# Optimization experiments

Hardware: AMD Instinct MI355X
Metric: run time of the kernel (lower is better)

The kernel has to match this reference:

```python
import jax, jax.numpy as jnp
import numpy as np
import math

# Static module config (matches init_kwargs)
C = 1.0            # ball curvature parameter c
IN_C, OUT_C = 512, 512
K, PAD = 3, 1
T, B = 2048, 16
EPS = 1e-15
RC = math.sqrt(C)

def _beta(a, b):
    return math.exp(math.lgamma(a) + math.lgamma(b) - math.lgamma(a + b))

BETA_NI = _beta(IN_C / 2.0, 0.5)            # beta(n_i/2, 1/2)
BETA_N = _beta(IN_C * K / 2.0, 0.5)         # beta(n/2, 1/2)
BETA_RATIO = BETA_N / BETA_NI
PROJ_EPS = 4e-3                              # geoopt float32 projection eps


def logmap0(y):
    # y in Poincare ball -> tangent at origin
    yn = jnp.clip(jnp.linalg.norm(y, axis=-1, keepdims=True), EPS, None)
    arg = jnp.clip(RC * yn, None, 1.0 - 1e-7)
    return y * (jnp.arctanh(arg) / (RC * yn))


def expmap0(u):
    un = jnp.clip(jnp.linalg.norm(u, axis=-1, keepdims=True), EPS, None)
    return jnp.tanh(RC * un) * u / (RC * un)


def project(x):
    maxnorm = (1.0 - PROJ_EPS) / RC
    norm = jnp.clip(jnp.linalg.norm(x, axis=-1, keepdims=True), EPS, None)
    return x * jnp.where(norm > maxnorm, maxnorm / norm, 1.0)


def poincare_linear(x, w_g, w_unit, b):
    # unidirectional Poincare MLR (geoopt_plusplus)
    rcx = RC * x                                             # [T,B,K*Cin]
    cx2 = jnp.sum(rcx * rcx, axis=-1, keepdims=True)         # [T,B,1]
    drcr = 2.0 * RC * b                                      # [Cout]
    num = 2.0 * jnp.einsum('tbi,io->tbo', rcx, w_unit) * jnp.cosh(drcr) \
          - (1.0 + cx2) * jnp.sinh(drcr)
    y = (2.0 * w_g / RC) * jnp.arcsinh(num / jnp.clip(1.0 - cx2, EPS, None))
    y = jnp.sinh(RC * y) / RC
    denom = 1.0 + jnp.sqrt(1.0 + C * jnp.sum(y * y, axis=-1, keepdims=True))
    return project(y / denom)


def setup_inputs() -> dict:
    key = jax.random.key(0)
    k1, k2, k3 = jax.random.split(key, 3)
    # points strictly inside the unit ball: ||x|| < 0.7
    v = jax.random.normal(k1, (T, B, IN_C), dtype=jnp.float32)
    vn = jnp.linalg.norm(v, axis=-1, keepdims=True)
    x = v / (1.0 + vn) * 0.7
    std = (2.0 * IN_C * K * OUT_C) ** -0.5
    w = jax.random.normal(k2, (K * IN_C, OUT_C), dtype=jnp.float32) * std
    weight_g = jnp.clip(jnp.linalg.norm(w, axis=0), 1e-15, None)   # [Cout]
    weight_v = w / weight_g                                        # [K*Cin, Cout]
    bias = jnp.zeros((OUT_C,), dtype=jnp.float32)
    return {"x": x, "weight_g": weight_g, "weight_v": weight_v, "bias": bias}


def reference(x, weight_g, weight_v, bias):
    u = logmap0(x) * BETA_RATIO                 # tangent space, rescaled
    u = jnp.pad(u, ((PAD, PAD), (0, 0), (0, 0)))
    olen = u.shape[0] - K + 1
    # im2col over time: [olen, B, K*Cin]
    u = jnp.concatenate([u[k:k + olen] for k in range(K)], axis=-1)
    xh = expmap0(u)
    w_unit = weight_v / jnp.clip(jnp.linalg.norm(weight_v, axis=0), EPS, None)
    return poincare_linear(xh, weight_g, w_unit, bias)
```

## Files before the change

### kernel.cpp

```cpp
#include <hip/hip_runtime.h>
#include <cstdint>
#include <cmath>

typedef unsigned short u16;
typedef short bf16x8 __attribute__((ext_vector_type(8)));
typedef float f32x4 __attribute__((ext_vector_type(4)));

#define T_DIM 2048
#define B_DIM 16
#define CIN 512
#define COUT 512
#define KIN 1536
#define NROWS (T_DIM * B_DIM)
#define UROWS ((T_DIM + 2) * B_DIM)

#define BM 128
#define BK 64
#define NT (KIN / BK)

#define LOG2E 1.44269504088896f
#define LN2   0.69314718055995f

__device__ __forceinline__ float fast_exp2(float x) {
#if __has_builtin(__builtin_amdgcn_exp2f)
  return __builtin_amdgcn_exp2f(x);
#else
  return __builtin_exp2f(x);
#endif
}
__device__ __forceinline__ float fast_log2(float x) {
#if __has_builtin(__builtin_amdgcn_logf)
  return __builtin_amdgcn_logf(x);
#else
  return __builtin_log2f(x);
#endif
}
__device__ __forceinline__ float fast_rcp(float x) {
  return __builtin_amdgcn_rcpf(x);
}

__device__ __forceinline__ u16 f2bf(float f) {
  unsigned u = __builtin_bit_cast(unsigned, f);
  u = (u + 0x7FFFu + ((u >> 16) & 1u)) >> 16;
  return (u16)u;
}

typedef __attribute__((address_space(3))) unsigned int as3u32;
typedef __attribute__((address_space(1))) unsigned int as1u32;

__device__ __forceinline__ void gload16(const u16* g, const u16* lds) {
#if __has_builtin(__builtin_amdgcn_global_load_lds)
  __builtin_amdgcn_global_load_lds((as1u32*)(uintptr_t)g,
                                   (as3u32*)(unsigned)(uintptr_t)lds, 16, 0, 0);
#else
  unsigned lane = __lane_id();
  ((uint4*)lds)[lane] = *(const uint4*)g;
#endif
}

__global__ __launch_bounds__(256) void k_colnorm(const float* __restrict__ wv,
                                                 float* __restrict__ partial) {
  int o = blockIdx.x * 256 + threadIdx.x;
  int r0 = blockIdx.y * 64;
  float s = 0.f;
#pragma unroll 8
  for (int r = 0; r < 64; ++r) {
    float v = wv[(size_t)(r0 + r) * COUT + o];
    s += v * v;
  }
  partial[(size_t)blockIdx.y * COUT + o] = s;
}

__global__ __launch_bounds__(256) void k_fin(const float* __restrict__ partial,
                                             float* __restrict__ invn) {
  int o = blockIdx.x * 256 + threadIdx.x;
  float s = 0.f;
#pragma unroll
  for (int j = 0; j < KIN / 64; ++j) s += partial[(size_t)j * COUT + o];
  invn[o] = 1.f / fmaxf(sqrtf(s), 1e-15f);
}

__global__ void k_chsh(const float* __restrict__ bias, float* __restrict__ ch,
                       float* __restrict__ sh) {
  int o = blockIdx.x * blockDim.x + threadIdx.x;
  if (o < COUT) {
    float d = 2.f * bias[o];
    float e = fast_exp2(d * LOG2E);
    float ie = fast_rcp(e);
    ch[o] = 0.5f * (e + ie);
    sh[o] = 0.5f * (e - ie);
  }
}

__global__ void k_wt(const float* __restrict__ wv, const float* __restrict__ invn,
                     u16* __restrict__ wt) {
  __shared__ float tile[64][65];
  int i0 = blockIdx.x * 64;
  int o0 = blockIdx.y * 64;
  int tx = threadIdx.x & 63, ty = threadIdx.x >> 6;
  for (int r = ty; r < 64; r += 4)
    tile[r][tx] = wv[(size_t)(i0 + r) * COUT + o0 + tx];
  __syncthreads();
  for (int r = ty; r < 64; r += 4) {
    float inv = invn[o0 + r];
    wt[(size_t)(o0 + r) * KIN + i0 + tx] = f2bf(tile[tx][r] * inv);
  }
}

__global__ void k_logmap(const float* __restrict__ x, u16* __restrict__ U,
                         float* __restrict__ nsq, float beta_ratio) {
  int row = blockIdx.x;
  int t = row >> 4;
  int lane = threadIdx.x;
  uint4* urow = (uint4*)(U + (size_t)row * CIN);
  if (t == 0 || t == T_DIM + 1) {
    uint4 z; z.x = z.y = z.z = z.w = 0u;
    urow[lane] = z;
    if (lane == 0) nsq[row] = 0.f;
    return;
  }
  const float4* xr = (const float4*)(x + (size_t)(row - 16) * CIN);
  float4 a = xr[lane * 2];
  float4 b = xr[lane * 2 + 1];
  float s = a.x*a.x + a.y*a.y + a.z*a.z + a.w*a.w
          + b.x*b.x + b.y*b.y + b.z*b.z + b.w*b.w;
#pragma unroll
  for (int d = 1; d < 64; d <<= 1) s += __shfl_xor(s, d);
  float r = sqrtf(s);
  float yn = fmaxf(r, 1e-15f);
  float arg = fminf(yn, 1.0f - 1e-7f);
  float at = 0.5f * LN2 * fast_log2((1.f + arg) * fast_rcp(1.f - arg));
  float f = at / yn * beta_ratio;
  union { u16 h[8]; uint4 v; } pk;
  pk.h[0] = f2bf(a.x * f); pk.h[1] = f2bf(a.y * f);
  pk.h[2] = f2bf(a.z * f); pk.h[3] = f2bf(a.w * f);
  pk.h[4] = f2bf(b.x * f); pk.h[5] = f2bf(b.y * f);
  pk.h[6] = f2bf(b.z * f); pk.h[7] = f2bf(b.w * f);
  urow[lane] = pk.v;
  if (lane == 0) nsq[row] = s * f * f;
}

__global__ __launch_bounds__(256) void k_rows(const float* __restrict__ nsq,
                                              float* __restrict__ R1,
                                              float* __restrict__ R2) {
  int m = blockIdx.x * 256 + threadIdx.x;
  float un2 = nsq[m] + nsq[m + 16] + nsq[m + 32];
  float un = sqrtf(un2);
  float unc = fmaxf(un, 1e-15f);
  float e2 = fast_exp2(unc * (2.f * LOG2E));
  float th = (e2 - 1.f) * fast_rcp(e2 + 1.f);
  float sxp = th * fast_rcp(unc);
  float cx2 = sxp * sxp * un2;
  float iden = fast_rcp(fmaxf(1.f - cx2, 1e-15f));
  R1[m] = 2.f * sxp * iden;
  R2[m] = (1.f + cx2) * iden;
}

__global__ __launch_bounds__(512, 2) void k_gemm(const u16* __restrict__ U,
                                                 const u16* __restrict__ WT,
                                                 const float* __restrict__ R1,
                                                 const float* __restrict__ R2,
                                                 const float* __restrict__ wg,
                                                 const float* __restrict__ chv,
                                                 const float* __restrict__ shv,
                                                 float* __restrict__ out) {
  __shared__ u16 lA[2][BM * BK];
  __shared__ u16 lB[COUT * BK];
  int bm = blockIdx.x;
  int tid = threadIdx.x;
  int lane = tid & 63;
  int wid = tid >> 6;
  int wr = wid >> 2, wc = wid & 3;
  int lr = lane & 15;
  int srow = tid >> 3;
  int chSw = (tid & 7) ^ (srow & 7);
  int pc0 = (((lane >> 4)) ^ (lr & 7)) << 3;
  int pc1 = (((lane >> 4) | 4) ^ (lr & 7)) << 3;

  f32x4 acc[4][8] = {};

  auto STAGE_A = [&](int t, int p) {
    int seg = t >> 3;
    int c0 = (t & 7) << 6;
    const u16* gA = U + (size_t)(bm * BM + seg * 16) * 512 + c0 + chSw * 8;
#pragma unroll
    for (int r = 0; r < 2; ++r) {
      int row = r * 64 + srow;
      gload16(gA + (size_t)row * 512, &lA[p][(r * 64 + wid * 8) * BK]);
    }
  };
  auto STAGE_B = [&](int t) {
    const u16* gB = WT + (size_t)t * 64 + chSw * 8;
#pragma unroll
    for (int r = 0; r < 8; ++r) {
      int row = r * 64 + srow;
      gload16(gB + (size_t)row * KIN, &lB[(r * 64 + wid * 8) * BK]);
    }
  };

  STAGE_A(0, 0);
  STAGE_B(0);
  asm volatile("s_waitcnt vmcnt(0)" ::: "memory");
  asm volatile("s_barrier" ::: "memory");

  for (int t = 0; t < NT; ++t) {
    int p = t & 1;
    if (t < NT - 1) STAGE_A(t + 1, p ^ 1);
    const u16* pA = &lA[p][(wr * 64 + lr) * BK];
    const u16* pB = &lB[(wc * 128 + lr) * BK];
#pragma unroll
    for (int kk = 0; kk < 2; ++kk) {
      int pc = kk ? pc1 : pc0;
      bf16x8 af[4], bf[8];
#pragma unroll
      for (int i = 0; i < 4; ++i) af[i] = *(const bf16x8*)(pA + i * 16 * BK + pc);
#pragma unroll
      for (int i = 0; i < 8; ++i) bf[i] = *(const bf16x8*)(pB + i * 16 * BK + pc);
      __builtin_amdgcn_s_setprio(1);
#pragma unroll
      for (int mi = 0; mi < 4; ++mi)
#pragma unroll
        for (int ni = 0; ni < 8; ++ni)
          acc[mi][ni] = __builtin_amdgcn_mfma_f32_16x16x32_bf16(
              af[mi], bf[ni], acc[mi][ni], 0, 0, 0);
      __builtin_amdgcn_s_setprio(0);
    }
    asm volatile("s_waitcnt lgkmcnt(0)" ::: "memory");
    asm volatile("s_barrier" ::: "memory");
    if (t < NT - 1) {
      STAGE_B(t + 1);
      asm volatile("s_waitcnt vmcnt(0)" ::: "memory");
      asm volatile("s_barrier" ::: "memory");
    }
  }
  float* scr = (float*)&lA[0][0];
  float* scl = scr + 128 * 4;

  float g8[8], c8[8], s8[8];
#pragma unroll
  for (int ni = 0; ni < 8; ++ni) {
    int col = wc * 128 + ni * 16 + lr;
    g8[ni] = wg[col]; c8[ni] = chv[col]; s8[ni] = shv[col];
  }

  int rbase_loc = wr * 64 + ((lane >> 4) << 2);
  int rbase_glb = bm * BM + rbase_loc;

#pragma unroll
  for (int mi = 0; mi < 4; ++mi) {
    float4 r1v = *(const float4*)(R1 + rbase_glb + mi * 16);
    float4 r2v = *(const float4*)(R2 + rbase_glb + mi * 16);
    float r1a[4] = {r1v.x, r1v.y, r1v.z, r1v.w};
    float r2a[4] = {r2v.x, r2v.y, r2v.z, r2v.w};
    float ssq[4] = {0.f, 0.f, 0.f, 0.f};
#pragma unroll
    for (int ni = 0; ni < 8; ++ni) {
#pragma unroll
      for (int j = 0; j < 4; ++j) {
        float z = r1a[j] * acc[mi][ni][j] * c8[ni] - r2a[j] * s8[ni];
        float w = z + sqrtf(fmaf(z, z, 1.f));
        float l = fast_log2(w);
        float E = fast_exp2((2.f * g8[ni]) * l);
        float y = 0.5f * (E - fast_rcp(E));
        acc[mi][ni][j] = y;
        ssq[j] += y * y;
      }
    }
#pragma unroll
    for (int j = 0; j < 4; ++j) {
#pragma unroll
      for (int d = 1; d < 16; d <<= 1) ssq[j] += __shfl_xor(ssq[j], d);
    }
    if (lr == 0) {
#pragma unroll
      for (int j = 0; j < 4; ++j)
        scr[(rbase_loc + mi * 16 + j) * 4 + wc] = ssq[j];
    }
  }
  __syncthreads();
  if (tid < 128) {
    float ss = scr[tid * 4] + scr[tid * 4 + 1] + scr[tid * 4 + 2] + scr[tid * 4 + 3];
    float denom = 1.f + sqrtf(1.f + ss);
    float idn = 1.f / denom;
    float nrm = fmaxf(sqrtf(ss) * idn, 1e-15f);
    float maxn = 1.0f - 4e-3f;
    float scale = (nrm > maxn) ? (maxn / nrm) : 1.f;
    scl[tid] = scale * idn;
  }
  __syncthreads();

#pragma unroll
  for (int mi = 0; mi < 4; ++mi) {
    float sc[4];
#pragma unroll
    for (int j = 0; j < 4; ++j) sc[j] = scl[rbase_loc + mi * 16 + j];
#pragma unroll
    for (int ni = 0; ni < 8; ++ni) {
      int col = wc * 128 + ni * 16 + lr;
#pragma unroll
      for (int j = 0; j < 4; ++j)
        out[(size_t)(rbase_glb + mi * 16 + j) * COUT + col] = acc[mi][ni][j] * sc[j];
    }
  }
}

extern "C" void kernel_launch(void* const* d_in, const int* in_sizes, int n_in,
                              void* d_out, int out_size, void* d_ws, size_t ws_size,
                              hipStream_t stream) {
  const float* x    = (const float*)d_in[0];
  const float* wg   = (const float*)d_in[1];
  const float* wv   = (const float*)d_in[2];
  const float* bias = (const float*)d_in[3];
  float* out = (float*)d_out;

  char* ws = (char*)d_ws;
  u16*   U    = (u16*)(ws);
  float* NSQ  = (float*)(ws + 33587200);
  u16*   WT   = (u16*)(ws + 33718400);
  float* INVN = (float*)(ws + 35291264);
  float* CH   = (float*)(ws + 35293312);
  float* SH   = (float*)(ws + 35295360);
  float* PART = (float*)(ws + 35297408);
  float* R1   = (float*)(ws + 35346560);
  float* R2   = (float*)(ws + 35477632);

  double lb = (lgamma(768.0) + lgamma(0.5) - lgamma(768.5))
            - (lgamma(256.0) + lgamma(0.5) - lgamma(256.5));
  float beta_ratio = (float)exp(lb);

  k_colnorm<<<dim3(COUT / 256, KIN / 64), 256, 0, stream>>>(wv, PART);
  k_fin<<<COUT / 256, 256, 0, stream>>>(PART, INVN);
  k_chsh<<<COUT / 128, 128, 0, stream>>>(bias, CH, SH);
  k_wt<<<dim3(KIN / 64, COUT / 64), 256, 0, stream>>>(wv, INVN, WT);
  k_logmap<<<UROWS, 64, 0, stream>>>(x, U, NSQ, beta_ratio);
  k_rows<<<NROWS / 256, 256, 0, stream>>>(NSQ, R1, R2);
  k_gemm<<<NROWS / BM, 512, 0, stream>>>(U, WT, R1, R2, wg, CH, SH, out);
}
```

Baseline: 116.7 us.

## Triple-buffer A and B tiles in GEMM and fold row/bias kernels into neighbors

The GEMM main loop moves from BK=64 with double-buffered A and a single B buffer (two barriers per step) to BK=32 with three rotating buffers for both A and B. Loads run two stages ahead and each step uses one barrier with a partial vmcnt wait. The k_rows kernel is removed and its per-row tanh/denominator math is recomputed in the GEMM epilogue from nsq. k_chsh is merged into k_fin, cutting two launches. The cost is three times as many pipeline steps with smaller MFMA bursts per barrier and some extra epilogue work.

```diff
diff --git a/kernel.cpp b/kernel.cpp
--- a/kernel.cpp
+++ b/kernel.cpp
@@ -14,9 +14,7 @@
 #define NROWS (T_DIM * B_DIM)
 #define UROWS ((T_DIM + 2) * B_DIM)
 
-#define BM 128
-#define BK 64
-#define NT (KIN / BK)
+#define NS 48
 
 #define LOG2E 1.44269504088896f
 #define LN2   0.69314718055995f
@@ -72,24 +70,20 @@
 }
 
 __global__ __launch_bounds__(256) void k_fin(const float* __restrict__ partial,
-                                             float* __restrict__ invn) {
+                                             const float* __restrict__ bias,
+                                             float* __restrict__ invn,
+                                             float* __restrict__ ch,
+                                             float* __restrict__ sh) {
   int o = blockIdx.x * 256 + threadIdx.x;
   float s = 0.f;
 #pragma unroll
   for (int j = 0; j < KIN / 64; ++j) s += partial[(size_t)j * COUT + o];
   invn[o] = 1.f / fmaxf(sqrtf(s), 1e-15f);
-}
-
-__global__ void k_chsh(const float* __restrict__ bias, float* __restrict__ ch,
-                       float* __restrict__ sh) {
-  int o = blockIdx.x * blockDim.x + threadIdx.x;
-  if (o < COUT) {
-    float d = 2.f * bias[o];
-    float e = fast_exp2(d * LOG2E);
-    float ie = fast_rcp(e);
-    ch[o] = 0.5f * (e + ie);
-    sh[o] = 0.5f * (e - ie);
-  }
+  float d = 2.f * bias[o];
+  float e = fast_exp2(d * LOG2E);
+  float ie = fast_rcp(e);
+  ch[o] = 0.5f * (e + ie);
+  sh[o] = 0.5f * (e - ie);
 }
 
 __global__ void k_wt(const float* __restrict__ wv, const float* __restrict__ invn,
@@ -140,82 +134,58 @@
   if (lane == 0) nsq[row] = s * f * f;
 }
 
-__global__ __launch_bounds__(256) void k_rows(const float* __restrict__ nsq,
-                                              float* __restrict__ R1,
-                                              float* __restrict__ R2) {
-  int m = blockIdx.x * 256 + threadIdx.x;
-  float un2 = nsq[m] + nsq[m + 16] + nsq[m + 32];
-  float un = sqrtf(un2);
-  float unc = fmaxf(un, 1e-15f);
-  float e2 = fast_exp2(unc * (2.f * LOG2E));
-  float th = (e2 - 1.f) * fast_rcp(e2 + 1.f);
-  float sxp = th * fast_rcp(unc);
-  float cx2 = sxp * sxp * un2;
-  float iden = fast_rcp(fmaxf(1.f - cx2, 1e-15f));
-  R1[m] = 2.f * sxp * iden;
-  R2[m] = (1.f + cx2) * iden;
-}
-
 __global__ __launch_bounds__(512, 2) void k_gemm(const u16* __restrict__ U,
                                                  const u16* __restrict__ WT,
-                                                 const float* __restrict__ R1,
-                                                 const float* __restrict__ R2,
+                                                 const float* __restrict__ nsq,
                                                  const float* __restrict__ wg,
                                                  const float* __restrict__ chv,
                                                  const float* __restrict__ shv,
                                                  float* __restrict__ out) {
-  __shared__ u16 lA[2][BM * BK];
-  __shared__ u16 lB[COUT * BK];
+  __shared__ u16 lA[3][128 * 32];
+  __shared__ u16 lB[3][512 * 32];
   int bm = blockIdx.x;
   int tid = threadIdx.x;
   int lane = tid & 63;
   int wid = tid >> 6;
   int wr = wid >> 2, wc = wid & 3;
   int lr = lane & 15;
-  int srow = tid >> 3;
-  int chSw = (tid & 7) ^ (srow & 7);
-  int pc0 = (((lane >> 4)) ^ (lr & 7)) << 3;
-  int pc1 = (((lane >> 4) | 4) ^ (lr & 7)) << 3;
+  int sc = (tid & 3) ^ ((tid >> 3) & 3);
+  int cSwz = ((lane >> 4) ^ ((lr >> 1) & 3)) << 3;
 
   f32x4 acc[4][8] = {};
 
-  auto STAGE_A = [&](int t, int p) {
-    int seg = t >> 3;
-    int c0 = (t & 7) << 6;
-    const u16* gA = U + (size_t)(bm * BM + seg * 16) * 512 + c0 + chSw * 8;
-#pragma unroll
-    for (int r = 0; r < 2; ++r) {
-      int row = r * 64 + srow;
-      gload16(gA + (size_t)row * 512, &lA[p][(r * 64 + wid * 8) * BK]);
-    }
+  auto stgA = [&](int t, int p) {
+    int seg = t >> 4;
+    int c0 = (t & 15) << 5;
+    gload16(U + (size_t)(bm * 128 + seg * 16 + (tid >> 2)) * 512 + c0 + sc * 8,
+            &lA[p][wid * 512]);
   };
-  auto STAGE_B = [&](int t) {
-    const u16* gB = WT + (size_t)t * 64 + chSw * 8;
-#pragma unroll
-    for (int r = 0; r < 8; ++r) {
-      int row = r * 64 + srow;
-      gload16(gB + (size_t)row * KIN, &lB[(r * 64 + wid * 8) * BK]);
-    }
+  auto stgB = [&](int t, int p) {
+#pragma unroll
+    for (int r = 0; r < 4; ++r)
+      gload16(WT + (size_t)(r * 128 + (tid >> 2)) * KIN + t * 32 + sc * 8,
+              &lB[p][r * 4096 + wid * 512]);
   };
 
-  STAGE_A(0, 0);
-  STAGE_B(0);
-  asm volatile("s_waitcnt vmcnt(0)" ::: "memory");
+  stgA(0, 0); stgB(0, 0);
+  stgA(1, 1); stgB(1, 1);
+  asm volatile("s_waitcnt vmcnt(5)" ::: "memory");
   asm volatile("s_barrier" ::: "memory");
 
-  for (int t = 0; t < NT; ++t) {
-    int p = t & 1;
-    if (t < NT - 1) STAGE_A(t + 1, p ^ 1);
-    const u16* pA = &lA[p][(wr * 64 + lr) * BK];
-    const u16* pB = &lB[(wc * 128 + lr) * BK];
-#pragma unroll
-    for (int kk = 0; kk < 2; ++kk) {
-      int pc = kk ? pc1 : pc0;
+  for (int tt = 0; tt < 16; ++tt) {
+#pragma unroll
+    for (int u = 0; u < 3; ++u) {
+      int t = tt * 3 + u;
+      int b = u;
+      int p = (u + 2) % 3;
+      if (t + 2 < NS) { stgA(t + 2, p); stgB(t + 2, p); }
+      const u16* pA = &lA[b][(wr * 64 + lr) * 32 + cSwz];
+      const u16* pB = &lB[b][(wc * 128 + lr) * 32 + cSwz];
       bf16x8 af[4], bf[8];
 #pragma unroll
-      for (int i = 0; i < 4; ++i) af[i] = *(const bf16x8*)(pA + i * 16 * BK + pc);
-#pragma unroll
-      for (int i = 0; i < 8; ++i) bf[i] = *(const bf16x8*)(pB + i * 16 * BK + pc);
+      for (int i = 0; i < 4; ++i) af[i] = *(const bf16x8*)(pA + i * 512);
+#pragma unroll
+      for (int i = 0; i < 8; ++i) bf[i] = *(const bf16x8*)(pB + i * 512);
       __builtin_amdgcn_s_setprio(1);
 #pragma unroll
       for (int mi = 0; mi < 4; ++mi)
@@ -224,15 +194,13 @@
           acc[mi][ni] = __builtin_amdgcn_mfma_f32_16x16x32_bf16(
               af[mi], bf[ni], acc[mi][ni], 0, 0, 0);
       __builtin_amdgcn_s_setprio(0);
-    }
-    asm volatile("s_waitcnt lgkmcnt(0)" ::: "memory");
-    asm volatile("s_barrier" ::: "memory");
-    if (t < NT - 1) {
-      STAGE_B(t + 1);
-      asm volatile("s_waitcnt vmcnt(0)" ::: "memory");
+      asm volatile("s_waitcnt lgkmcnt(0)" ::: "memory");
+      if (t < NS - 2)       asm volatile("s_waitcnt vmcnt(5)" ::: "memory");
+      else if (t == NS - 2) asm volatile("s_waitcnt vmcnt(0)" ::: "memory");
       asm volatile("s_barrier" ::: "memory");
     }
   }
+
   float* scr = (float*)&lA[0][0];
   float* scl = scr + 128 * 4;
 
@@ -242,17 +210,27 @@
     int col = wc * 128 + ni * 16 + lr;
     g8[ni] = wg[col]; c8[ni] = chv[col]; s8[ni] = shv[col];
   }
-
   int rbase_loc = wr * 64 + ((lane >> 4) << 2);
-  int rbase_glb = bm * BM + rbase_loc;
+  int rbase_glb = bm * 128 + rbase_loc;
 
 #pragma unroll
   for (int mi = 0; mi < 4; ++mi) {
-    float4 r1v = *(const float4*)(R1 + rbase_glb + mi * 16);
-    float4 r2v = *(const float4*)(R2 + rbase_glb + mi * 16);
-    float r1a[4] = {r1v.x, r1v.y, r1v.z, r1v.w};
-    float r2a[4] = {r2v.x, r2v.y, r2v.z, r2v.w};
-    float ssq[4] = {0.f, 0.f, 0.f, 0.f};
+    float r1a[4], r2a[4], ssq[4];
+#pragma unroll
+    for (int j = 0; j < 4; ++j) {
+      int m = rbase_glb + mi * 16 + j;
+      float un2 = nsq[m] + nsq[m + 16] + nsq[m + 32];
+      float un = sqrtf(un2);
+      float unc = fmaxf(un, 1e-15f);
+      float e2 = fast_exp2(unc * (2.f * LOG2E));
+      float th = (e2 - 1.f) * fast_rcp(e2 + 1.f);
+      float sxp = th * fast_rcp(unc);
+      float cx2 = sxp * sxp * un2;
+      float iden = fast_rcp(fmaxf(1.f - cx2, 1e-15f));
+      r1a[j] = 2.f * sxp * iden;
+      r2a[j] = (1.f + cx2) * iden;
+      ssq[j] = 0.f;
+    }
 #pragma unroll
     for (int ni = 0; ni < 8; ++ni) {
 #pragma unroll
@@ -291,15 +269,15 @@
 
 #pragma unroll
   for (int mi = 0; mi < 4; ++mi) {
-    float sc[4];
-#pragma unroll
-    for (int j = 0; j < 4; ++j) sc[j] = scl[rbase_loc + mi * 16 + j];
+    float sc4[4];
+#pragma unroll
+    for (int j = 0; j < 4; ++j) sc4[j] = scl[rbase_loc + mi * 16 + j];
 #pragma unroll
     for (int ni = 0; ni < 8; ++ni) {
       int col = wc * 128 + ni * 16 + lr;
 #pragma unroll
       for (int j = 0; j < 4; ++j)
-        out[(size_t)(rbase_glb + mi * 16 + j) * COUT + col] = acc[mi][ni][j] * sc[j];
+        out[(size_t)(rbase_glb + mi * 16 + j) * COUT + col] = acc[mi][ni][j] * sc4[j];
     }
   }
 }
@@ -321,18 +299,14 @@
   float* CH   = (float*)(ws + 35293312);
   float* SH   = (float*)(ws + 35295360);
   float* PART = (float*)(ws + 35297408);
-  float* R1   = (float*)(ws + 35346560);
-  float* R2   = (float*)(ws + 35477632);
 
   double lb = (lgamma(768.0) + lgamma(0.5) - lgamma(768.5))
             - (lgamma(256.0) + lgamma(0.5) - lgamma(256.5));
   float beta_ratio = (float)exp(lb);
 
   k_colnorm<<<dim3(COUT / 256, KIN / 64), 256, 0, stream>>>(wv, PART);
-  k_fin<<<COUT / 256, 256, 0, stream>>>(PART, INVN);
-  k_chsh<<<COUT / 128, 128, 0, stream>>>(bias, CH, SH);
+  k_fin<<<COUT / 256, 256, 0, stream>>>(PART, bias, INVN, CH, SH);
   k_wt<<<dim3(KIN / 64, COUT / 64), 256, 0, stream>>>(wv, INVN, WT);
   k_logmap<<<UROWS, 64, 0, stream>>>(x, U, NSQ, beta_ratio);
-  k_rows<<<NROWS / 256, 256, 0, stream>>>(NSQ, R1, R2);
-  k_gemm<<<NROWS / BM, 512, 0, stream>>>(U, WT, R1, R2, wg, CH, SH, out);
-}
+  k_gemm<<<NROWS / 128, 512, 0, stream>>>(U, WT, NSQ, wg, CH, SH, out);
+}
```

Result: faster. 105.0 us (-10.1%).
